# Performance work log

Measured on AMD Instinct MI355X. Metric: run time of the kernel, lower is better.

## Reference

```python
import jax, jax.numpy as jnp
import numpy as np

EPS = 1e-6

def rmsnorm(x, w):
    v = jnp.mean(jnp.square(x), axis=-1, keepdims=True)
    return x * jax.lax.rsqrt(v + EPS) * w

def setup_inputs() -> dict:
    key = jax.random.key(0)
    ks = jax.random.split(key, 12)
    H, Di, L = 2048, 4096, 1024   # hidden, mamba inner (expand*H), seq tokens
    DT, N, K = 128, 16, 4         # dt_rank, d_state, d_conv
    F = 8192                      # MLP intermediate
    s = lambda k, shp, sc: jax.random.normal(k, shp, jnp.float32) * sc
    return dict(
        hidden_states=s(ks[0], (L, H), 1.0),
        in_ln_w=jnp.ones((H,), jnp.float32),
        pre_ff_ln_w=jnp.ones((H,), jnp.float32),
        in_proj_w=s(ks[1], (2 * Di, H), 0.02),
        conv_w=s(ks[2], (Di, K), 0.1),
        conv_b=s(ks[3], (Di,), 0.1),
        x_proj_w=s(ks[4], (DT + 2 * N, Di), 0.02),
        dt_ln_w=jnp.ones((DT,), jnp.float32),
        b_ln_w=jnp.ones((N,), jnp.float32),
        c_ln_w=jnp.ones((N,), jnp.float32),
        dt_proj_w=s(ks[5], (Di, DT), 0.02),
        dt_proj_b=s(ks[6], (Di,), 0.1),
        A=-jnp.exp(jax.random.uniform(ks[7], (Di, N), jnp.float32, -4.0, 0.0)),
        D=jnp.ones((Di,), jnp.float32),
        out_proj_w=s(ks[8], (H, Di), 0.02),
        gate_up_w=s(ks[9], (2 * F, H), 0.02),
        down_w=s(ks[10], (H, F), 0.02),
    )

def reference(hidden_states, in_ln_w, pre_ff_ln_w, in_proj_w, conv_w, conv_b,
              x_proj_w, dt_ln_w, b_ln_w, c_ln_w, dt_proj_w, dt_proj_b,
              A, D, out_proj_w, gate_up_w, down_w):
    residual = hidden_states
    x = rmsnorm(hidden_states, in_ln_w)
    # --- Mamba mixer (prefill / selective_scan path) ---
    proj = x @ in_proj_w.T                          # [L, 2*Di]
    Di = in_proj_w.shape[0] // 2
    h, gate = proj[:, :Di], proj[:, Di:]
    # causal depthwise conv1d, kernel K, left pad K-1, then silu
    K = conv_w.shape[1]
    L = h.shape[0]
    hp = jnp.pad(h, ((K - 1, 0), (0, 0)))           # [L+K-1, Di]
    idx = jnp.arange(L)[:, None] + jnp.arange(K)[None, :]
    h = jnp.einsum('lkd,dk->ld', hp[idx], conv_w) + conv_b
    h = jax.nn.silu(h)
    # ssm parameters
    ssm = h @ x_proj_w.T                            # [L, DT+2N]
    DTr = dt_ln_w.shape[0]
    N = b_ln_w.shape[0]
    dt = rmsnorm(ssm[:, :DTr], dt_ln_w)
    B = rmsnorm(ssm[:, DTr:DTr + N], b_ln_w)
    C = rmsnorm(ssm[:, DTr + N:], c_ln_w)
    delta = jax.nn.softplus(dt @ dt_proj_w.T + dt_proj_b)   # [L, Di]
    # selective scan (discretize then linear recurrence over L)
    dA = jnp.exp(delta[:, :, None] * A[None, :, :])         # [L, Di, N]
    dBu = delta[:, :, None] * B[:, None, :] * h[:, :, None] # [L, Di, N]
    def step(s, inp):
        da, dbu = inp
        s = da * s + dbu
        return s, s
    s0 = jnp.zeros((Di, N), jnp.float32)
    _, states = jax.lax.scan(step, s0, (dA, dBu))           # [L, Di, N]
    y = jnp.einsum('ldn,ln->ld', states, C) + h * D
    y = y * jax.nn.silu(gate)
    mixer_out = y @ out_proj_w.T                    # [L, H]
    # --- residual + pre-FF norm + gated MLP ---
    residual = residual + mixer_out
    x = rmsnorm(residual, pre_ff_ln_w)
    gu = x @ gate_up_w.T                            # [L, 2F]
    F = down_w.shape[1]
    x = jax.nn.silu(gu[:, :F]) * gu[:, F:]
    ff = x @ down_w.T
    return residual + ff
```

## Files before the change

kernel.cpp:

```cpp
#include <hip/hip_runtime.h>
#include <math.h>

typedef unsigned short u16;
typedef __bf16 bf16x8 __attribute__((ext_vector_type(8)));
typedef short s16x8 __attribute__((ext_vector_type(8)));
typedef short s16x4 __attribute__((ext_vector_type(4)));
typedef float f32x4 __attribute__((ext_vector_type(4)));

__device__ __forceinline__ u16 f2bf(float f) {
  union { float f; unsigned u; } v; v.f = f;
  unsigned u = v.u;
  unsigned r = u + 0x7fffu + ((u >> 16) & 1u);
  return (u16)(r >> 16);
}
__device__ __forceinline__ float bf2f(u16 h) {
  union { unsigned u; float f; } v; v.u = ((unsigned)h) << 16;
  return v.f;
}
__device__ __forceinline__ float fast_softplus(float x) {
  return (x > 20.f) ? x : __logf(1.f + __expf(x));
}
__device__ __forceinline__ float fast_sig(float x) {
  return __builtin_amdgcn_rcpf(1.f + __expf(-x));
}

__device__ __forceinline__ void gld_lds16(const u16* g, u16* l) {
  __builtin_amdgcn_global_load_lds(
      (const __attribute__((address_space(1))) unsigned int*)g,
      (__attribute__((address_space(3))) unsigned int*)l, 16, 0, 0);
}

__global__ __launch_bounds__(256)
void f32_to_bf16_k(const float* __restrict__ src, u16* __restrict__ dst,
                   int n, int n_valid) {
  int i = (blockIdx.x * 256 + threadIdx.x) * 4;
  if (i >= n) return;
  s16x4 o;
  if (i + 3 < n_valid) {
    float4 v = *(const float4*)(src + i);
    o[0] = (short)f2bf(v.x); o[1] = (short)f2bf(v.y);
    o[2] = (short)f2bf(v.z); o[3] = (short)f2bf(v.w);
  } else {
    o[0] = 0; o[1] = 0; o[2] = 0; o[3] = 0;
  }
  *(s16x4*)(dst + i) = o;
}

template <int BN, int MODE, int SPLITK>
__global__ __launch_bounds__(256)
void gemm2(const u16* __restrict__ A, const u16* __restrict__ B,
           float* __restrict__ C, u16* __restrict__ Cb,
           const u16* __restrict__ aux, int M, int Nc, int K) {
  constexpr int NJ = BN / 32;
  constexpr int BISS = BN / 32;
  __shared__ __align__(16) u16 As[64 * 64];
  __shared__ __align__(16) u16 Bs[BN * 64];
  const int tid = threadIdx.x;
  const int tm0 = blockIdx.y * 64;
  const int tn0 = blockIdx.x * BN;
  const int kslice = K / SPLITK;
  const int k0 = blockIdx.z * kslice;
  const int wave = tid >> 6;
  const int lane = tid & 63;
  const int wm = (wave >> 1) * 32;
  const int wn = (wave & 1) * (BN / 2);
  const int frow = lane & 15;
  const int fc = lane >> 4;
  const int rmask = frow & 7;

  const int r0 = tid >> 3;
  const int csw = (((tid & 7) ^ (r0 & 7)) << 3);
  const u16* gA = A + (size_t)(tm0 + r0) * K + k0 + csw;
  const u16* gB = B + (size_t)(tn0 + r0) * K + k0 + csw;
  u16* lA = &As[tid * 8];
  u16* lB = &Bs[tid * 8];

  f32x4 acc[2][NJ];
  f32x4 zero = {0.f, 0.f, 0.f, 0.f};
#pragma unroll
  for (int i = 0; i < 2; ++i)
#pragma unroll
    for (int j = 0; j < NJ; ++j) acc[i][j] = zero;

  for (int kt = 0; kt < kslice; kt += 64) {
    __syncthreads();
    gld_lds16(gA, lA);
    gld_lds16(gA + (size_t)32 * K, lA + 2048);
#pragma unroll
    for (int b = 0; b < BISS; ++b)
      gld_lds16(gB + (size_t)32 * b * K, lB + b * 2048);
    gA += 64; gB += 64;
    __syncthreads();
#pragma unroll
    for (int s = 0; s < 2; ++s) {
      bf16x8 af[2], bfr[NJ];
#pragma unroll
      for (int i = 0; i < 2; ++i) {
        int addr = (wm + i * 16 + frow) * 64 + (((s * 4 + fc) ^ rmask) << 3);
        af[i] = __builtin_bit_cast(bf16x8, *(const s16x8*)&As[addr]);
      }
#pragma unroll
      for (int j = 0; j < NJ; ++j) {
        int addr = (wn + j * 16 + frow) * 64 + (((s * 4 + fc) ^ rmask) << 3);
        bfr[j] = __builtin_bit_cast(bf16x8, *(const s16x8*)&Bs[addr]);
      }
#pragma unroll
      for (int i = 0; i < 2; ++i)
#pragma unroll
        for (int j = 0; j < NJ; ++j)
          acc[i][j] = __builtin_amdgcn_mfma_f32_16x16x32_bf16(af[i], bfr[j], acc[i][j], 0, 0, 0);
    }
  }
  const int ccol = lane & 15;
  const int crow = (lane >> 4) * 4;
  float* Cp = C + (size_t)blockIdx.z * ((size_t)M * Nc);
#pragma unroll
  for (int i = 0; i < 2; ++i) {
#pragma unroll
    for (int j = 0; j < NJ; ++j) {
      int gn = tn0 + wn + j * 16 + ccol;
      if (gn < Nc) {
        size_t base = (size_t)(tm0 + wm + i * 16 + crow) * Nc + gn;
#pragma unroll
        for (int r = 0; r < 4; ++r) {
          float c = acc[i][j][r];
          size_t idx = base + (size_t)r * Nc;
          if (MODE == 0) {
            Cp[idx] = c;
          } else if (MODE == 1) {
            Cb[idx] = f2bf(c * fast_sig(c));
          } else {
            Cb[idx] = f2bf(c * bf2f(aux[idx]));
          }
        }
      }
    }
  }
}

template <int MODE, int SPLITK>
__global__ __launch_bounds__(256)
void gemm128(const u16* __restrict__ A, const u16* __restrict__ B,
             float* __restrict__ C, u16* __restrict__ Cb,
             const u16* __restrict__ aux, int M, int Nc, int K) {
  __shared__ __align__(16) u16 As[2 * 128 * 64];
  __shared__ __align__(16) u16 Bs[2 * 128 * 64];
  const int tid = threadIdx.x;
  const int tm0 = blockIdx.y * 128;
  const int tn0 = blockIdx.x * 128;
  const int kslice = K / SPLITK;
  const int k0 = blockIdx.z * kslice;
  const int wave = tid >> 6;
  const int lane = tid & 63;
  const int wm = (wave >> 1) * 64;
  const int wn = (wave & 1) * 64;
  const int frow = lane & 15;
  const int fc = lane >> 4;
  const int rmask = frow & 7;

  const int r0 = tid >> 3;
  const int csw = (((tid & 7) ^ (r0 & 7)) << 3);
  const u16* gA = A + (size_t)(tm0 + r0) * K + k0 + csw;
  const u16* gB = B + (size_t)(tn0 + r0) * K + k0 + csw;
  u16* lA = &As[tid * 8];
  u16* lB = &Bs[tid * 8];

  f32x4 acc[4][4];
  f32x4 zero = {0.f, 0.f, 0.f, 0.f};
#pragma unroll
  for (int i = 0; i < 4; ++i)
#pragma unroll
    for (int j = 0; j < 4; ++j) acc[i][j] = zero;

#pragma unroll
  for (int b = 0; b < 4; ++b) {
    gld_lds16(gA + (size_t)(32 * b) * K, lA + b * 2048);
    gld_lds16(gB + (size_t)(32 * b) * K, lB + b * 2048);
  }
  gA += 64; gB += 64;
  __syncthreads();

  const int nt = kslice >> 6;
  int buf = 0;
  for (int kt = 0; kt < nt; ++kt) {
    const int nb = buf ^ 1;
    if (kt + 1 < nt) {
#pragma unroll
      for (int b = 0; b < 4; ++b) {
        gld_lds16(gA + (size_t)(32 * b) * K, lA + nb * 8192 + b * 2048);
        gld_lds16(gB + (size_t)(32 * b) * K, lB + nb * 8192 + b * 2048);
      }
      gA += 64; gB += 64;
    }
    __builtin_amdgcn_sched_barrier(0);
    const int boff = buf * 8192;
#pragma unroll
    for (int s = 0; s < 2; ++s) {
      bf16x8 af[4], bfr[4];
#pragma unroll
      for (int i = 0; i < 4; ++i) {
        int addr = boff + (wm + i * 16 + frow) * 64 + (((s * 4 + fc) ^ rmask) << 3);
        af[i] = __builtin_bit_cast(bf16x8, *(const s16x8*)&As[addr]);
      }
#pragma unroll
      for (int j = 0; j < 4; ++j) {
        int addr = boff + (wn + j * 16 + frow) * 64 + (((s * 4 + fc) ^ rmask) << 3);
        bfr[j] = __builtin_bit_cast(bf16x8, *(const s16x8*)&Bs[addr]);
      }
#pragma unroll
      for (int i = 0; i < 4; ++i)
#pragma unroll
        for (int j = 0; j < 4; ++j)
          acc[i][j] = __builtin_amdgcn_mfma_f32_16x16x32_bf16(af[i], bfr[j], acc[i][j], 0, 0, 0);
    }
    __syncthreads();
    buf = nb;
  }

  const int ccol = lane & 15;
  const int crow = (lane >> 4) * 4;
  float* Cp = C + (size_t)blockIdx.z * ((size_t)M * Nc);
#pragma unroll
  for (int i = 0; i < 4; ++i) {
#pragma unroll
    for (int j = 0; j < 4; ++j) {
      int gn = tn0 + wn + j * 16 + ccol;
      size_t base = (size_t)(tm0 + wm + i * 16 + crow) * Nc + gn;
#pragma unroll
      for (int r = 0; r < 4; ++r) {
        float c = acc[i][j][r];
        size_t idx = base + (size_t)r * Nc;
        if (MODE == 0) {
          Cp[idx] = c;
        } else if (MODE == 1) {
          Cb[idx] = f2bf(c * fast_sig(c));
        } else {
          Cb[idx] = f2bf(c * bf2f(aux[idx]));
        }
      }
    }
  }
}

__device__ inline float block_reduce_sum_256(float v) {
  __shared__ float red[4];
  int lane = threadIdx.x & 63, wave = threadIdx.x >> 6;
#pragma unroll
  for (int m = 32; m > 0; m >>= 1) v += __shfl_xor(v, m, 64);
  if (lane == 0) red[wave] = v;
  __syncthreads();
  return red[0] + red[1] + red[2] + red[3];
}

__global__ __launch_bounds__(256)
void rmsnorm2048_k(const float* __restrict__ x, const float* __restrict__ w,
                   u16* __restrict__ y) {
  const int C = 2048;
  const int row = blockIdx.x;
  const int t = threadIdx.x;
  const float4* xr = (const float4*)(x + (size_t)row * C);
  float4 v0 = xr[t];
  float4 v1 = xr[t + 256];
  float ss = v0.x * v0.x + v0.y * v0.y + v0.z * v0.z + v0.w * v0.w +
             v1.x * v1.x + v1.y * v1.y + v1.z * v1.z + v1.w * v1.w;
  float tot = block_reduce_sum_256(ss);
  float sc = rsqrtf(tot * (1.0f / C) + 1e-6f);
  const float4* wr = (const float4*)w;
  float4 w0 = wr[t], w1 = wr[t + 256];
  u16* yr = y + (size_t)row * C;
  s16x4 o0, o1;
  o0[0] = (short)f2bf(v0.x * sc * w0.x); o0[1] = (short)f2bf(v0.y * sc * w0.y);
  o0[2] = (short)f2bf(v0.z * sc * w0.z); o0[3] = (short)f2bf(v0.w * sc * w0.w);
  o1[0] = (short)f2bf(v1.x * sc * w1.x); o1[1] = (short)f2bf(v1.y * sc * w1.y);
  o1[2] = (short)f2bf(v1.z * sc * w1.z); o1[3] = (short)f2bf(v1.w * sc * w1.w);
  *(s16x4*)(yr + t * 4) = o0;
  *(s16x4*)(yr + 1024 + t * 4) = o1;
}

__global__ __launch_bounds__(256)
void add_rmsnorm4_k(const float* __restrict__ a, const float* __restrict__ p,
                    const float* __restrict__ w, float* __restrict__ resid,
                    u16* __restrict__ y) {
  const int C = 2048;
  const size_t S = (size_t)1024 * 2048;
  const int row = blockIdx.x;
  const int t = threadIdx.x;
  const float4* ar = (const float4*)(a + (size_t)row * C);
  float4 v0 = ar[t], v1 = ar[t + 256];
#pragma unroll
  for (int s = 0; s < 4; ++s) {
    const float4* br = (const float4*)(p + s * S + (size_t)row * C);
    float4 u0 = br[t], u1 = br[t + 256];
    v0.x += u0.x; v0.y += u0.y; v0.z += u0.z; v0.w += u0.w;
    v1.x += u1.x; v1.y += u1.y; v1.z += u1.z; v1.w += u1.w;
  }
  float4* rr = (float4*)(resid + (size_t)row * C);
  rr[t] = v0; rr[t + 256] = v1;
  float ss = v0.x * v0.x + v0.y * v0.y + v0.z * v0.z + v0.w * v0.w +
             v1.x * v1.x + v1.y * v1.y + v1.z * v1.z + v1.w * v1.w;
  float tot = block_reduce_sum_256(ss);
  float sc = rsqrtf(tot * (1.0f / C) + 1e-6f);
  const float4* wr = (const float4*)w;
  float4 w0 = wr[t], w1 = wr[t + 256];
  u16* yr = y + (size_t)row * C;
  s16x4 o0, o1;
  o0[0] = (short)f2bf(v0.x * sc * w0.x); o0[1] = (short)f2bf(v0.y * sc * w0.y);
  o0[2] = (short)f2bf(v0.z * sc * w0.z); o0[3] = (short)f2bf(v0.w * sc * w0.w);
  o1[0] = (short)f2bf(v1.x * sc * w1.x); o1[1] = (short)f2bf(v1.y * sc * w1.y);
  o1[2] = (short)f2bf(v1.z * sc * w1.z); o1[3] = (short)f2bf(v1.w * sc * w1.w);
  *(s16x4*)(yr + t * 4) = o0;
  *(s16x4*)(yr + 1024 + t * 4) = o1;
}

__global__ __launch_bounds__(256)
void conv_silu_k(const float* __restrict__ proj, const float* __restrict__ cw,
                 const float* __restrict__ cb, u16* __restrict__ h) {
  const int Di = 4096, LD = 8192;
  int idx = blockIdx.x * 256 + threadIdx.x;
  int d = idx & (Di - 1);
  int l = idx >> 12;
  float4 w = *(const float4*)(cw + (size_t)d * 4);
  float acc = cb[d];
  int ls0 = l - 3;
  if (ls0 >= 0) acc += proj[(size_t)ls0 * LD + d] * w.x;
  if (ls0 + 1 >= 0) acc += proj[(size_t)(ls0 + 1) * LD + d] * w.y;
  if (ls0 + 2 >= 0) acc += proj[(size_t)(ls0 + 2) * LD + d] * w.z;
  acc += proj[(size_t)l * LD + d] * w.w;
  h[idx] = f2bf(acc * fast_sig(acc));
}

__global__ __launch_bounds__(64)
void ssm_norm_k(const float* __restrict__ ssmp, const float* __restrict__ dtw,
                const float* __restrict__ bw, const float* __restrict__ cw,
                u16* __restrict__ dtn, float* __restrict__ Bn,
                float* __restrict__ Cn) {
  const size_t S = (size_t)1024 * 160;
  int l = blockIdx.x;
  int lane = threadIdx.x;
  float d0 = 0.f, d1 = 0.f, bv = 0.f, cv = 0.f;
#pragma unroll
  for (int s = 0; s < 4; ++s) {
    const float* r = ssmp + s * S + (size_t)l * 160;
    d0 += r[lane];
    d1 += r[lane + 64];
    if (lane < 16) {
      bv += r[128 + lane];
      cv += r[144 + lane];
    }
  }
  float sd = d0 * d0 + d1 * d1;
  float sb = bv * bv;
  float sc = cv * cv;
#pragma unroll
  for (int m = 32; m > 0; m >>= 1) {
    sd += __shfl_xor(sd, m, 64);
    sb += __shfl_xor(sb, m, 64);
    sc += __shfl_xor(sc, m, 64);
  }
  float scd = rsqrtf(sd * (1.f / 128.f) + 1e-6f);
  float scb = rsqrtf(sb * (1.f / 16.f) + 1e-6f);
  float scc = rsqrtf(sc * (1.f / 16.f) + 1e-6f);
  dtn[(size_t)l * 128 + lane] = f2bf(d0 * scd * dtw[lane]);
  dtn[(size_t)l * 128 + lane + 64] = f2bf(d1 * scd * dtw[lane + 64]);
  if (lane < 16) {
    Bn[(size_t)l * 16 + lane] = bv * scb * bw[lane];
    Cn[(size_t)l * 16 + lane] = cv * scc * cw[lane];
  }
}

#define NCH 32
#define CHL 32

__global__ __launch_bounds__(256)
void scan_p1(const float* __restrict__ dpre, const float* __restrict__ dtb,
             const u16* __restrict__ h, const float* __restrict__ Bn,
             const float* __restrict__ Amat,
             float* __restrict__ carryA, float* __restrict__ carryS) {
  const int Di = 4096;
  int chunk = blockIdx.x & (NCH - 1);
  int d = (blockIdx.x >> 5) * 256 + threadIdx.x;
  __shared__ float Bs[CHL * 16];
  for (int i = threadIdx.x; i < CHL * 16; i += 256)
    Bs[i] = Bn[(size_t)chunk * CHL * 16 + i];
  __syncthreads();
  float a[16];
#pragma unroll
  for (int q = 0; q < 4; ++q)
    *(float4*)&a[q * 4] = *(const float4*)(Amat + (size_t)d * 16 + q * 4);
  float bias = dtb[d];
  float s[16];
#pragma unroll
  for (int n = 0; n < 16; ++n) s[n] = 0.f;
  float sumdel = 0.f;
  int l0 = chunk * CHL;
#pragma unroll 4
  for (int j = 0; j < CHL; ++j) {
    int l = l0 + j;
    float del = fast_softplus(dpre[(size_t)l * Di + d] + bias);
    float hv = bf2f(h[(size_t)l * Di + d]);
    sumdel += del;
    float c = del * hv;
#pragma unroll
    for (int n = 0; n < 16; ++n) {
      float dA = __expf(del * a[n]);
      s[n] = dA * s[n] + c * Bs[j * 16 + n];
    }
  }
  size_t base = (size_t)chunk * 65536 + (size_t)d * 16;
#pragma unroll
  for (int n = 0; n < 16; ++n) {
    carryA[base + n] = __expf(sumdel * a[n]);
    carryS[base + n] = s[n];
  }
}

__global__ __launch_bounds__(256)
void scan_p2(const float* __restrict__ carryA, float* __restrict__ carryS) {
  int p = blockIdx.x * 256 + threadIdx.x;
  float cin = 0.f;
#pragma unroll
  for (int c = 0; c < NCH; ++c) {
    float av = carryA[(size_t)c * 65536 + p];
    float sv = carryS[(size_t)c * 65536 + p];
    float nx = av * cin + sv;
    carryS[(size_t)c * 65536 + p] = cin;
    cin = nx;
  }
}

__global__ __launch_bounds__(256)
void scan_p3(const float* __restrict__ dpre, const float* __restrict__ dtb,
             const u16* __restrict__ h, const float* __restrict__ Bn,
             const float* __restrict__ Cn, const float* __restrict__ Amat,
             const float* __restrict__ Dw, const float* __restrict__ proj,
             const float* __restrict__ carryS, u16* __restrict__ y) {
  const int Di = 4096;
  int chunk = blockIdx.x & (NCH - 1);
  int d = (blockIdx.x >> 5) * 256 + threadIdx.x;
  __shared__ float Bs[CHL * 16];
  __shared__ float Cs[CHL * 16];
  for (int i = threadIdx.x; i < CHL * 16; i += 256) {
    Bs[i] = Bn[(size_t)chunk * CHL * 16 + i];
    Cs[i] = Cn[(size_t)chunk * CHL * 16 + i];
  }
  __syncthreads();
  float a[16];
#pragma unroll
  for (int q = 0; q < 4; ++q)
    *(float4*)&a[q * 4] = *(const float4*)(Amat + (size_t)d * 16 + q * 4);
  float bias = dtb[d];
  float Dd = Dw[d];
  float s[16];
  size_t base = (size_t)chunk * 65536 + (size_t)d * 16;
#pragma unroll
  for (int q = 0; q < 4; ++q)
    *(float4*)&s[q * 4] = *(const float4*)(carryS + base + q * 4);
  int l0 = chunk * CHL;
#pragma unroll 2
  for (int j = 0; j < CHL; ++j) {
    int l = l0 + j;
    float del = fast_softplus(dpre[(size_t)l * Di + d] + bias);
    float hv = bf2f(h[(size_t)l * Di + d]);
    float c = del * hv;
    float p = 0.f;
#pragma unroll
    for (int n = 0; n < 16; ++n) {
      float dA = __expf(del * a[n]);
      s[n] = dA * s[n] + c * Bs[j * 16 + n];
      p += s[n] * Cs[j * 16 + n];
    }
    float g = proj[(size_t)l * 8192 + 4096 + d];
    float yv = p + hv * Dd;
    y[(size_t)l * Di + d] = f2bf(yv * g * fast_sig(g));
  }
}

__global__ __launch_bounds__(256)
void add4_k(float* __restrict__ out, const float* __restrict__ p) {
  const size_t S = (size_t)1024 * 2048;
  int i = blockIdx.x * 256 + threadIdx.x;
  float4 a = ((const float4*)out)[i];
#pragma unroll
  for (int s = 0; s < 4; ++s) {
    float4 b = ((const float4*)(p + s * S))[i];
    a.x += b.x; a.y += b.y; a.z += b.z; a.w += b.w;
  }
  ((float4*)out)[i] = a;
}

extern "C" void kernel_launch(void* const* d_in, const int* in_sizes, int n_in,
                              void* d_out, int out_size, void* d_ws, size_t ws_size,
                              hipStream_t stream) {
  const float* hidden      = (const float*)d_in[0];
  const float* in_ln_w     = (const float*)d_in[1];
  const float* pre_ff_ln_w = (const float*)d_in[2];
  const float* in_proj_w   = (const float*)d_in[3];
  const float* conv_w      = (const float*)d_in[4];
  const float* conv_b      = (const float*)d_in[5];
  const float* x_proj_w    = (const float*)d_in[6];
  const float* dt_ln_w     = (const float*)d_in[7];
  const float* b_ln_w      = (const float*)d_in[8];
  const float* c_ln_w      = (const float*)d_in[9];
  const float* dt_proj_w   = (const float*)d_in[10];
  const float* dt_proj_b   = (const float*)d_in[11];
  const float* Amat        = (const float*)d_in[12];
  const float* Dw          = (const float*)d_in[13];
  const float* out_proj_w  = (const float*)d_in[14];
  const float* gate_up_w   = (const float*)d_in[15];
  const float* down_w      = (const float*)d_in[16];
  float* out = (float*)d_out;
  float* ws = (float*)d_ws;

  const int L = 1024, H = 2048, Di = 4096, F = 8192;

  u16*   wbuf   = (u16*)ws;
  float* carryA = ws + 2097152;
  float* carryS = ws + 4194304;
  float* proj   = ws + 8388608;
  float* dpre   = ws + 16777216;
  float* ssmp   = ws + 16777216;
  u16*   hbuf   = (u16*)(ws + 20971520);
  u16*   xnorm  = (u16*)(ws + 23068672);
  u16*   dtn    = (u16*)(ws + 24281088);
  float* Bn     = ws + 24346624;
  float* Cn     = ws + 24363008;
  u16*   ybuf   = (u16*)(ws + 24379392);
  float* mixp   = ws + 8388608;
  u16*   x2     = (u16*)(ws + 18874368);
  u16*   sg     = (u16*)(ws + 8388608);
  u16*   x3     = (u16*)(ws + 12582912);
  float* ffp    = ws + 16777216;

  rmsnorm2048_k<<<L, 256, 0, stream>>>(hidden, in_ln_w, xnorm);
  f32_to_bf16_k<<<16384, 256, 0, stream>>>(in_proj_w, wbuf, 16777216, 16777216);
  gemm128<0, 1><<<dim3(64, 8), 256, 0, stream>>>(xnorm, wbuf, proj, nullptr, nullptr, L, 8192, 2048);
  conv_silu_k<<<(L * Di) / 256, 256, 0, stream>>>(proj, conv_w, conv_b, hbuf);
  f32_to_bf16_k<<<1024, 256, 0, stream>>>(x_proj_w, wbuf, 1048576, 655360);
  gemm2<64, 0, 4><<<dim3(4, 16, 4), 256, 0, stream>>>(hbuf, wbuf, ssmp, nullptr, nullptr, L, 160, 4096);
  ssm_norm_k<<<L, 64, 0, stream>>>(ssmp, dt_ln_w, b_ln_w, c_ln_w, dtn, Bn, Cn);
  f32_to_bf16_k<<<512, 256, 0, stream>>>(dt_proj_w, wbuf, 524288, 524288);
  gemm2<128, 0, 1><<<dim3(32, 16), 256, 0, stream>>>(dtn, wbuf, dpre, nullptr, nullptr, L, 4096, 128);
  scan_p1<<<16 * NCH, 256, 0, stream>>>(dpre, dt_proj_b, hbuf, Bn, Amat, carryA, carryS);
  scan_p2<<<256, 256, 0, stream>>>(carryA, carryS);
  scan_p3<<<16 * NCH, 256, 0, stream>>>(dpre, dt_proj_b, hbuf, Bn, Cn, Amat, Dw, proj, carryS, ybuf);
  f32_to_bf16_k<<<8192, 256, 0, stream>>>(out_proj_w, wbuf, 8388608, 8388608);
  gemm128<0, 4><<<dim3(16, 8, 4), 256, 0, stream>>>(ybuf, wbuf, mixp, nullptr, nullptr, L, 2048, 4096);
  add_rmsnorm4_k<<<L, 256, 0, stream>>>(hidden, mixp, pre_ff_ln_w, out, x2);
  f32_to_bf16_k<<<16384, 256, 0, stream>>>(gate_up_w, wbuf, 16777216, 16777216);
  gemm128<1, 1><<<dim3(64, 8), 256, 0, stream>>>(x2, wbuf, nullptr, sg, nullptr, L, 8192, 2048);
  f32_to_bf16_k<<<16384, 256, 0, stream>>>(gate_up_w + 16777216, wbuf, 16777216, 16777216);
  gemm128<2, 1><<<dim3(64, 8), 256, 0, stream>>>(x2, wbuf, nullptr, x3, sg, L, 8192, 2048);
  f32_to_bf16_k<<<16384, 256, 0, stream>>>(down_w, wbuf, 16777216, 16777216);
  gemm128<0, 4><<<dim3(16, 8, 4), 256, 0, stream>>>(x3, wbuf, ffp, nullptr, nullptr, L, 2048, 8192);
  add4_k<<<(L * H / 4) / 256, 256, 0, stream>>>(out, ffp);
}
```

Before: 632.0 us.

## Double-buffer gemm2 LDS tiles and use partial vmcnt waits in both GEMMs

Gives the smaller gemm2 kernel double-buffered LDS tiles so the next K tile loads while MFMAs consume the current one. Both GEMM kernels swap __syncthreads for explicit s_waitcnt vmcnt(N) plus s_barrier, waiting only on the previous stage's loads and leaving the newest prefetch in flight. This raises LDS use in gemm2 and relies on hand-counted outstanding-load numbers. If those counts are wrong, the result is a race.

```diff
diff --git a/kernel.cpp b/kernel.cpp
--- a/kernel.cpp
+++ b/kernel.cpp
@@ -53,8 +53,10 @@
            const u16* __restrict__ aux, int M, int Nc, int K) {
   constexpr int NJ = BN / 32;
   constexpr int BISS = BN / 32;
-  __shared__ __align__(16) u16 As[64 * 64];
-  __shared__ __align__(16) u16 Bs[BN * 64];
+  constexpr int ABUF = 64 * 64;
+  constexpr int BBUF = BN * 64;
+  __shared__ __align__(16) u16 As[2 * ABUF];
+  __shared__ __align__(16) u16 Bs[2 * BBUF];
   const int tid = threadIdx.x;
   const int tm0 = blockIdx.y * 64;
   const int tn0 = blockIdx.x * BN;
@@ -82,26 +84,41 @@
 #pragma unroll
     for (int j = 0; j < NJ; ++j) acc[i][j] = zero;
 
-  for (int kt = 0; kt < kslice; kt += 64) {
-    __syncthreads();
-    gld_lds16(gA, lA);
-    gld_lds16(gA + (size_t)32 * K, lA + 2048);
+  auto stage = [&](int bi) {
+    gld_lds16(gA, lA + bi * ABUF);
+    gld_lds16(gA + (size_t)32 * K, lA + bi * ABUF + 2048);
 #pragma unroll
     for (int b = 0; b < BISS; ++b)
-      gld_lds16(gB + (size_t)32 * b * K, lB + b * 2048);
+      gld_lds16(gB + (size_t)32 * b * K, lB + bi * BBUF + b * 2048);
     gA += 64; gB += 64;
-    __syncthreads();
+  };
+
+  stage(0);
+  const int nt = kslice >> 6;
+  int buf = 0;
+  for (int kt = 0; kt < nt; ++kt) {
+    const int nb = buf ^ 1;
+    if (kt + 1 < nt) {
+      stage(nb);
+      if constexpr (BN == 64) asm volatile("s_waitcnt vmcnt(4)" ::: "memory");
+      else                    asm volatile("s_waitcnt vmcnt(6)" ::: "memory");
+    } else {
+      asm volatile("s_waitcnt vmcnt(0)" ::: "memory");
+    }
+    __builtin_amdgcn_s_barrier();
+    __builtin_amdgcn_sched_barrier(0);
+    const int ao = buf * ABUF, bo = buf * BBUF;
 #pragma unroll
     for (int s = 0; s < 2; ++s) {
       bf16x8 af[2], bfr[NJ];
 #pragma unroll
       for (int i = 0; i < 2; ++i) {
-        int addr = (wm + i * 16 + frow) * 64 + (((s * 4 + fc) ^ rmask) << 3);
+        int addr = ao + (wm + i * 16 + frow) * 64 + (((s * 4 + fc) ^ rmask) << 3);
         af[i] = __builtin_bit_cast(bf16x8, *(const s16x8*)&As[addr]);
       }
 #pragma unroll
       for (int j = 0; j < NJ; ++j) {
-        int addr = (wn + j * 16 + frow) * 64 + (((s * 4 + fc) ^ rmask) << 3);
+        int addr = bo + (wn + j * 16 + frow) * 64 + (((s * 4 + fc) ^ rmask) << 3);
         bfr[j] = __builtin_bit_cast(bf16x8, *(const s16x8*)&Bs[addr]);
       }
 #pragma unroll
@@ -110,6 +127,8 @@
         for (int j = 0; j < NJ; ++j)
           acc[i][j] = __builtin_amdgcn_mfma_f32_16x16x32_bf16(af[i], bfr[j], acc[i][j], 0, 0, 0);
     }
+    __builtin_amdgcn_s_barrier();
+    buf = nb;
   }
   const int ccol = lane & 15;
   const int crow = (lane >> 4) * 4;
@@ -172,26 +191,27 @@
 #pragma unroll
     for (int j = 0; j < 4; ++j) acc[i][j] = zero;
 
-#pragma unroll
-  for (int b = 0; b < 4; ++b) {
-    gld_lds16(gA + (size_t)(32 * b) * K, lA + b * 2048);
-    gld_lds16(gB + (size_t)(32 * b) * K, lB + b * 2048);
-  }
-  gA += 64; gB += 64;
-  __syncthreads();
-
+  auto stage = [&](int bi) {
+#pragma unroll
+    for (int b = 0; b < 4; ++b) {
+      gld_lds16(gA + (size_t)(32 * b) * K, lA + bi * 8192 + b * 2048);
+      gld_lds16(gB + (size_t)(32 * b) * K, lB + bi * 8192 + b * 2048);
+    }
+    gA += 64; gB += 64;
+  };
+
+  stage(0);
   const int nt = kslice >> 6;
   int buf = 0;
   for (int kt = 0; kt < nt; ++kt) {
     const int nb = buf ^ 1;
     if (kt + 1 < nt) {
-#pragma unroll
-      for (int b = 0; b < 4; ++b) {
-        gld_lds16(gA + (size_t)(32 * b) * K, lA + nb * 8192 + b * 2048);
-        gld_lds16(gB + (size_t)(32 * b) * K, lB + nb * 8192 + b * 2048);
-      }
-      gA += 64; gB += 64;
-    }
+      stage(nb);
+      asm volatile("s_waitcnt vmcnt(8)" ::: "memory");
+    } else {
+      asm volatile("s_waitcnt vmcnt(0)" ::: "memory");
+    }
+    __builtin_amdgcn_s_barrier();
     __builtin_amdgcn_sched_barrier(0);
     const int boff = buf * 8192;
 #pragma unroll
@@ -213,7 +233,7 @@
         for (int j = 0; j < 4; ++j)
           acc[i][j] = __builtin_amdgcn_mfma_f32_16x16x32_bf16(af[i], bfr[j], acc[i][j], 0, 0, 0);
     }
-    __syncthreads();
+    __builtin_amdgcn_s_barrier();
     buf = nb;
   }
 
```

Result: no change. 636.7 us (+0.7%).
